# Kernel optimization log

Hardware: AMD Instinct MI355X
Metric: run time of the kernel (lower is better)

The kernel has to match this reference:

```python
import jax, jax.numpy as jnp
import numpy as np

IN_FEATURES = 512
OUT_FEATURES = 512
GRID_SIZE = 5
SPLINE_ORDER = 3
GRID_RANGE = (-3.0, 3.0)


def make_grid():
    h = (GRID_RANGE[1] - GRID_RANGE[0]) / GRID_SIZE
    g = jnp.arange(-SPLINE_ORDER, GRID_SIZE + SPLINE_ORDER + 1, dtype=jnp.float32) * h + GRID_RANGE[0]
    return jnp.broadcast_to(g, (IN_FEATURES, g.shape[0]))  # [in, grid_size+2*order+1]


def b_splines(x, grid):
    # x: [N, in] -> bases: [N, in, grid_size + spline_order]
    x = x[..., None]  # [N, in, 1]
    bases = ((x >= grid[:, :-1]) & (x < grid[:, 1:])).astype(x.dtype)
    for k in range(1, SPLINE_ORDER + 1):
        left = (x - grid[:, :-(k + 1)]) / (grid[:, k:-1] - grid[:, :-(k + 1)])
        right = (grid[:, k + 1:] - x) / (grid[:, k + 1:] - grid[:, 1:-k])
        bases = left * bases[..., :-1] + right * bases[..., 1:]
    return bases


def setup_inputs() -> dict:
    key = jax.random.key(0)
    k1, k2, k3, k4 = jax.random.split(key, 4)
    N = 32768
    bound = 1.0 / np.sqrt(IN_FEATURES)  # kaiming_uniform-ish scale
    x = jax.random.normal(k1, (N, IN_FEATURES), dtype=jnp.float32)
    base_weight = jax.random.uniform(k2, (OUT_FEATURES, IN_FEATURES), minval=-bound, maxval=bound, dtype=jnp.float32)
    spline_weight = jax.random.normal(k3, (OUT_FEATURES, IN_FEATURES, GRID_SIZE + SPLINE_ORDER), dtype=jnp.float32) * 0.1
    spline_scaler = jax.random.uniform(k4, (OUT_FEATURES, IN_FEATURES), minval=-bound, maxval=bound, dtype=jnp.float32)
    grid = make_grid()
    return {"x": x, "base_weight": base_weight, "spline_weight": spline_weight, "spline_scaler": spline_scaler, "grid": grid}


def reference(x, base_weight, spline_weight, spline_scaler, grid):
    # base branch: SiLU(x) @ W_base^T
    base_out = jnp.einsum('ni,oi->no', jax.nn.silu(x), base_weight)
    # spline branch: Cox-de Boor basis then GEMM with scaled spline weights
    b = b_splines(x, grid)  # [N, in, G+K]
    sw = spline_weight * spline_scaler[..., None]  # [out, in, G+K]
    spline_out = jnp.einsum('nik,oik->no', b, sw)
    return base_out + spline_out
```

## Files before the change

kernel.cpp:

```cpp
#include <hip/hip_runtime.h>

#define NSAMP 32768
#define INF 512
#define OUTF 512
#define NB 8
#define KSP 4096
#define KTOT 4608

typedef __attribute__((ext_vector_type(8))) short bf16x8;
typedef __attribute__((ext_vector_type(4))) float f32x4;

typedef __attribute__((address_space(1))) void gas_void;
typedef __attribute__((address_space(3))) void las_void;
#define GLL16(g, l) __builtin_amdgcn_global_load_lds( \
    (const gas_void*)(g), (las_void*)(l), 16, 0, 0)

__device__ __forceinline__ unsigned short f2bf(float f) {
  unsigned int u = __float_as_uint(f);
  u += 0x7fffu + ((u >> 16) & 1u);
  return (unsigned short)(u >> 16);
}

__device__ __forceinline__ unsigned pack_rn(float lo, float hi) {
  return __builtin_amdgcn_perm(__float_as_uint(hi) + 0x8000u,
                               __float_as_uint(lo) + 0x8000u, 0x07060302u);
}

__device__ __forceinline__ uint4 kan_basis_vec(float xv) {
  float t = __builtin_fmaf(xv, 1.0f / 1.2f, 5.5f);
  float cf = floorf(t);
  float u = t - cf;
  int j0 = (int)cf - 3;
  float omu = 1.0f - u;
  float u2 = u * u, u3 = u2 * u;
  float omu2 = omu * omu;
  float w0 = omu2 * omu;
  float w1 = __builtin_fmaf(3.f, u3, __builtin_fmaf(-6.f, u2, 4.f));
  float w2 = __builtin_fmaf(-3.f, u3,
              __builtin_fmaf(3.f, u2, __builtin_fmaf(3.f, u, 1.f)));
  float w3 = u3;
  unsigned P0 = pack_rn(w0, w1);
  unsigned P1 = pack_rn(w2, w3);
  int p = j0 & 1;
  unsigned Q0 = p ? (P0 << 16) : P0;
  unsigned Q1 = p ? __builtin_amdgcn_alignbit(P1, P0, 16) : P1;
  unsigned Q2 = p ? (P1 >> 16) : 0u;
  int D = j0 >> 1;
  uint4 r;
  r.x = (D == 0) ? Q0 : (D == -1) ? Q1 : (D == -2) ? Q2 : 0u;
  r.y = (D == 1) ? Q0 : (D ==  0) ? Q1 : (D == -1) ? Q2 : 0u;
  r.z = (D == 2) ? Q0 : (D ==  1) ? Q1 : (D ==  0) ? Q2 : 0u;
  r.w = (D == 3) ? Q0 : (D ==  2) ? Q1 : (D ==  1) ? Q2 : 0u;
  return r;
}

__global__ __launch_bounds__(256) void kan_prep_w(
    const float* __restrict__ bw, const float* __restrict__ sw,
    const float* __restrict__ sc, unsigned short* __restrict__ W) {
  int idx = blockIdx.x * 256 + threadIdx.x;
  float scv = sc[idx] * (1.0f / 6.0f);
  float4 s0 = ((const float4*)sw)[idx * 2 + 0];
  float4 s1 = ((const float4*)sw)[idx * 2 + 1];
  unsigned short v[8];
  v[0] = f2bf(s0.x * scv); v[1] = f2bf(s0.y * scv);
  v[2] = f2bf(s0.z * scv); v[3] = f2bf(s0.w * scv);
  v[4] = f2bf(s1.x * scv); v[5] = f2bf(s1.y * scv);
  v[6] = f2bf(s1.z * scv); v[7] = f2bf(s1.w * scv);
  int o = idx >> 9, i = idx & 511;
  *(bf16x8*)(W + (size_t)o * KTOT + i * NB) = *(bf16x8*)v;
  W[(size_t)o * KTOT + KSP + i] = f2bf(bw[idx]);
}

__device__ __forceinline__ void mfma16(
    f32x4 acc[4][8], const bf16x8 av[4], const bf16x8 bv[4], int nh) {
  #pragma unroll
  for (int mf = 0; mf < 4; ++mf)
    #pragma unroll
    for (int g = 0; g < 4; ++g)
      acc[mf][nh * 4 + g] = __builtin_amdgcn_mfma_f32_16x16x32_bf16(
          av[mf], bv[g], acc[mf][nh * 4 + g], 0, 0, 0);
}

__global__ __launch_bounds__(256, 2) void kan_fused(
    const float* __restrict__ x, const unsigned short* __restrict__ W,
    float* __restrict__ out) {
  __shared__ __align__(16) unsigned short As[128 * 64];
  __shared__ __align__(16) unsigned short Bs[2][256 * 64];
  const int tid = threadIdx.x;
  const int wave = tid >> 6;
  const int lane = tid & 63;
  const int frow = lane & 15;
  const int quad = lane >> 4;
  const int lr = lane >> 3;
  const int lc = lane & 7;
  const int mtile = blockIdx.x & 255;
  const int ntile = blockIdx.x >> 8;
  const int wm = (wave & 1) << 6;
  const int wn = (wave >> 1) << 7;
  const int fr7 = frow & 7;
  const int sa0 = (quad ^ fr7) * 8;
  const int sa1 = ((4 + quad) ^ fr7) * 8;

  f32x4 acc[4][8];
  #pragma unroll
  for (int i = 0; i < 4; ++i)
    #pragma unroll
    for (int j = 0; j < 8; ++j)
      acc[i][j] = (f32x4){0.f, 0.f, 0.f, 0.f};

  const unsigned short* bg = W +
      (size_t)(ntile * 256 + wave * 64 + lr) * KTOT + ((lc ^ lr) * 8);
  const float* xb = x + (size_t)mtile * 128 * INF;
  const float* xp[4];
  #pragma unroll
  for (int is = 0; is < 4; ++is)
    xp[is] = xb + (size_t)(wave * 32 + is * 8 + lr) * INF + lc;

  {
    float xc[4];
    #pragma unroll
    for (int is = 0; is < 4; ++is) xc[is] = xp[is][0];
    #pragma unroll
    for (int is = 0; is < 8; ++is)
      GLL16(bg + is * 36864, &Bs[0][(wave * 64 + is * 8) * 64]);
    bg += 64;
    #pragma unroll
    for (int is = 0; is < 4; ++is) {
      uint4 bb = kan_basis_vec(xc[is]);
      *(uint4*)&As[(wave * 32 + is * 8 + lr) * 64 + ((lc ^ lr) * 8)] = bb;
    }
    asm volatile("s_waitcnt vmcnt(0)");
    __syncthreads();
  }

  for (int kc = 0; kc < 72; ++kc) {
    const unsigned short* Bc = Bs[kc & 1];
    unsigned short* Bn = (unsigned short*)Bs[(kc + 1) & 1];
    bf16x8 av[4], bv[4];
    float xn[4];
    float4 v0[4], v1[4];

    if (kc < 63) {
      #pragma unroll
      for (int is = 0; is < 4; ++is) xn[is] = xp[is][(kc + 1) * 8];
    }
    if (kc < 71) {
      #pragma unroll
      for (int is = 0; is < 8; ++is)
        GLL16(bg + is * 36864, &Bn[(wave * 64 + is * 8) * 64]);
      bg += 64;
    }
    #pragma unroll
    for (int f = 0; f < 4; ++f)
      av[f] = *(const bf16x8*)&As[(wm + f * 16 + frow) * 64 + sa0];
    #pragma unroll
    for (int g = 0; g < 4; ++g)
      bv[g] = *(const bf16x8*)&Bc[(wn + g * 16 + frow) * 64 + sa0];
    __builtin_amdgcn_s_barrier();
    asm volatile("s_waitcnt lgkmcnt(0)");
    __builtin_amdgcn_sched_barrier(0);
    __builtin_amdgcn_s_setprio(1);
    mfma16(acc, av, bv, 0);
    __builtin_amdgcn_s_setprio(0);
    __builtin_amdgcn_s_barrier();

    #pragma unroll
    for (int g = 0; g < 4; ++g)
      bv[g] = *(const bf16x8*)&Bc[(wn + (g + 4) * 16 + frow) * 64 + sa0];
    __builtin_amdgcn_s_barrier();
    asm volatile("s_waitcnt lgkmcnt(0)");
    __builtin_amdgcn_sched_barrier(0);
    __builtin_amdgcn_s_setprio(1);
    mfma16(acc, av, bv, 1);
    __builtin_amdgcn_s_setprio(0);
    __builtin_amdgcn_s_barrier();

    if (kc >= 63 && kc < 71) {
      const int scn = kc - 63;
      #pragma unroll
      for (int is = 0; is < 4; ++is) {
        const float* xr =
            xb + (size_t)(wave * 32 + is * 8 + lr) * INF + scn * 64 + lc * 8;
        v0[is] = *(const float4*)xr;
        v1[is] = *(const float4*)(xr + 4);
      }
    }
    #pragma unroll
    for (int f = 0; f < 4; ++f)
      av[f] = *(const bf16x8*)&As[(wm + f * 16 + frow) * 64 + sa1];
    #pragma unroll
    for (int g = 0; g < 4; ++g)
      bv[g] = *(const bf16x8*)&Bc[(wn + g * 16 + frow) * 64 + sa1];
    __builtin_amdgcn_s_barrier();
    asm volatile("s_waitcnt lgkmcnt(0)");
    __builtin_amdgcn_sched_barrier(0);
    __builtin_amdgcn_s_setprio(1);
    mfma16(acc, av, bv, 0);
    __builtin_amdgcn_s_setprio(0);
    __builtin_amdgcn_s_barrier();

    #pragma unroll
    for (int g = 0; g < 4; ++g)
      bv[g] = *(const bf16x8*)&Bc[(wn + (g + 4) * 16 + frow) * 64 + sa1];
    if (kc < 63) {
      #pragma unroll
      for (int is = 0; is < 4; ++is) {
        uint4 bb = kan_basis_vec(xn[is]);
        *(uint4*)&As[(wave * 32 + is * 8 + lr) * 64 + ((lc ^ lr) * 8)] = bb;
      }
    } else if (kc < 71) {
      #pragma unroll
      for (int is = 0; is < 4; ++is) {
        float vv[8] = {v0[is].x, v0[is].y, v0[is].z, v0[is].w,
                       v1[is].x, v1[is].y, v1[is].z, v1[is].w};
        float s[8];
        #pragma unroll
        for (int e = 0; e < 8; ++e)
          s[e] = vv[e] * __builtin_amdgcn_rcpf(1.0f + __expf(-vv[e]));
        uint4 pk;
        pk.x = pack_rn(s[0], s[1]);
        pk.y = pack_rn(s[2], s[3]);
        pk.z = pack_rn(s[4], s[5]);
        pk.w = pack_rn(s[6], s[7]);
        *(uint4*)&As[(wave * 32 + is * 8 + lr) * 64 + ((lc ^ lr) * 8)] = pk;
      }
    }
    if (kc < 71)
      asm volatile("s_waitcnt vmcnt(0)");
    __builtin_amdgcn_s_barrier();
    asm volatile("s_waitcnt lgkmcnt(0)");
    __builtin_amdgcn_sched_barrier(0);
    __builtin_amdgcn_s_setprio(1);
    mfma16(acc, av, bv, 1);
    __builtin_amdgcn_s_setprio(0);
    __builtin_amdgcn_s_barrier();
  }

  const size_t m0 = (size_t)mtile * 128;
  const int n0 = ntile * 256;
  #pragma unroll
  for (int mf = 0; mf < 4; ++mf)
    #pragma unroll
    for (int nf = 0; nf < 8; ++nf)
      #pragma unroll
      for (int r = 0; r < 4; ++r)
        out[(m0 + wm + mf * 16 + quad * 4 + r) * OUTF + (n0 + wn + nf * 16 + frow)] =
            acc[mf][nf][r];
}

__global__ __launch_bounds__(256) void kan_naive(
    const float* __restrict__ x, const float* __restrict__ bw,
    const float* __restrict__ sw, const float* __restrict__ sc,
    float* __restrict__ out) {
  int idx = blockIdx.x * 256 + threadIdx.x;
  int n = idx >> 9, o = idx & 511;
  const float* xr = x + (size_t)n * INF;
  float acc = 0.f;
  for (int i = 0; i < INF; ++i) {
    float xv = xr[i];
    float sil = xv / (1.0f + __expf(-xv));
    float t = (xv + 6.6f) * (1.0f / 1.2f);
    float cf = floorf(t);
    float u = t - cf;
    int j0 = (int)cf - 3;
    float omu = 1.0f - u;
    float u2 = u * u, u3 = u2 * u;
    float w[4];
    w[0] = (1.0f / 6.0f) * omu * omu * omu;
    w[1] = (1.0f / 6.0f) * (3.0f * u3 - 6.0f * u2 + 4.0f);
    w[2] = (1.0f / 6.0f) * (-3.0f * u3 + 3.0f * u2 + 3.0f * u + 1.0f);
    w[3] = (1.0f / 6.0f) * u3;
    int wi = o * INF + i;
    acc += sil * bw[wi];
    float sp = 0.f;
    #pragma unroll
    for (int m = 0; m < 4; ++m) {
      int j = j0 + m;
      if ((unsigned)j < 8u) sp += w[m] * sw[wi * NB + j];
    }
    acc += sp * sc[wi];
  }
  out[idx] = acc;
}

extern "C" void kernel_launch(void* const* d_in, const int* in_sizes, int n_in,
                              void* d_out, int out_size, void* d_ws, size_t ws_size,
                              hipStream_t stream) {
  const float* x  = (const float*)d_in[0];
  const float* bw = (const float*)d_in[1];
  const float* sw = (const float*)d_in[2];
  const float* sc = (const float*)d_in[3];
  float* out = (float*)d_out;

  const size_t wbytes = (size_t)OUTF * KTOT * 2;
  if (ws_size >= wbytes) {
    unsigned short* W = (unsigned short*)d_ws;
    kan_prep_w<<<(OUTF * INF) / 256, 256, 0, stream>>>(bw, sw, sc, W);
    kan_fused<<<(NSAMP / 128) * (OUTF / 256), 256, 0, stream>>>(x, W, out);
  } else {
    kan_naive<<<(NSAMP * OUTF) / 256, 256, 0, stream>>>(x, bw, sw, sc, out);
  }
}
```

Baseline: 268.7 us.

## Enlarge fused KAN GEMM tile to 256x256 with 8 waves and double-buffered A

The fused kernel moves from 128x256 tiles with 4 waves to 256x256 tiles with 8 waves (512 threads). Each wave now computes a 128x64 sub-tile, and the A tile (spline basis / SiLU values) is double-buffered in shared memory. Basis computation and B-tile global-to-LDS loads are spread across the four MFMA phases of each K step. The aim is more reuse of each loaded W tile, fewer blocks, and better overlap of basis generation with MFMA. The cost is 64KB of LDS per block, which likely limits occupancy below the declared two blocks per CU, plus heavier per-thread register pressure.

```diff
diff --git a/kernel.cpp b/kernel.cpp
--- a/kernel.cpp
+++ b/kernel.cpp
@@ -72,19 +72,19 @@
 }
 
 __device__ __forceinline__ void mfma16(
-    f32x4 acc[4][8], const bf16x8 av[4], const bf16x8 bv[4], int nh) {
+    f32x4 acc[8][4], int mbase, const bf16x8 av[4], const bf16x8 bv[4]) {
   #pragma unroll
   for (int mf = 0; mf < 4; ++mf)
     #pragma unroll
     for (int g = 0; g < 4; ++g)
-      acc[mf][nh * 4 + g] = __builtin_amdgcn_mfma_f32_16x16x32_bf16(
-          av[mf], bv[g], acc[mf][nh * 4 + g], 0, 0, 0);
-}
-
-__global__ __launch_bounds__(256, 2) void kan_fused(
+      acc[mbase + mf][g] = __builtin_amdgcn_mfma_f32_16x16x32_bf16(
+          av[mf], bv[g], acc[mbase + mf][g], 0, 0, 0);
+}
+
+__global__ __launch_bounds__(512, 2) void kan_fused(
     const float* __restrict__ x, const unsigned short* __restrict__ W,
     float* __restrict__ out) {
-  __shared__ __align__(16) unsigned short As[128 * 64];
+  __shared__ __align__(16) unsigned short As[2][256 * 64];
   __shared__ __align__(16) unsigned short Bs[2][256 * 64];
   const int tid = threadIdx.x;
   const int wave = tid >> 6;
@@ -93,159 +93,194 @@
   const int quad = lane >> 4;
   const int lr = lane >> 3;
   const int lc = lane & 7;
-  const int mtile = blockIdx.x & 255;
-  const int ntile = blockIdx.x >> 8;
-  const int wm = (wave & 1) << 6;
-  const int wn = (wave >> 1) << 7;
+  const int mtile = blockIdx.x & 127;
+  const int ntile = blockIdx.x >> 7;
+  const int wm = (wave & 1) << 7;
+  const int wn = (wave >> 1) << 6;
   const int fr7 = frow & 7;
   const int sa0 = (quad ^ fr7) * 8;
   const int sa1 = ((4 + quad) ^ fr7) * 8;
 
-  f32x4 acc[4][8];
+  f32x4 acc[8][4];
   #pragma unroll
-  for (int i = 0; i < 4; ++i)
-    #pragma unroll
-    for (int j = 0; j < 8; ++j)
+  for (int i = 0; i < 8; ++i)
+    #pragma unroll
+    for (int j = 0; j < 4; ++j)
       acc[i][j] = (f32x4){0.f, 0.f, 0.f, 0.f};
 
   const unsigned short* bg = W +
-      (size_t)(ntile * 256 + wave * 64 + lr) * KTOT + ((lc ^ lr) * 8);
-  const float* xb = x + (size_t)mtile * 128 * INF;
-  const float* xp[4];
-  #pragma unroll
-  for (int is = 0; is < 4; ++is)
-    xp[is] = xb + (size_t)(wave * 32 + is * 8 + lr) * INF + lc;
+      (size_t)(ntile * 256 + wave * 8 + lr) * KTOT + ((lc ^ lr) * 8);
+  const float* xb = x + (size_t)mtile * 256 * INF;
+  const int rt = tid >> 1;
+  const int half = tid & 1;
+  const int rt7 = rt & 7;
+  const float* xs_sp = xb + (size_t)rt * INF + half * 4;
+  const float* xs_si = xb + (size_t)rt * INF + half * 32;
 
   {
-    float xc[4];
-    #pragma unroll
-    for (int is = 0; is < 4; ++is) xc[is] = xp[is][0];
-    #pragma unroll
-    for (int is = 0; is < 8; ++is)
-      GLL16(bg + is * 36864, &Bs[0][(wave * 64 + is * 8) * 64]);
+    float4 xv = *(const float4*)xs_sp;
+    #pragma unroll
+    for (int ir = 0; ir < 4; ++ir)
+      GLL16(bg + (size_t)ir * (64 * KTOT), &Bs[0][(ir * 64 + wave * 8) * 64]);
     bg += 64;
-    #pragma unroll
-    for (int is = 0; is < 4; ++is) {
-      uint4 bb = kan_basis_vec(xc[is]);
-      *(uint4*)&As[(wave * 32 + is * 8 + lr) * 64 + ((lc ^ lr) * 8)] = bb;
-    }
-    asm volatile("s_waitcnt vmcnt(0)");
+    float xe[4] = {xv.x, xv.y, xv.z, xv.w};
+    #pragma unroll
+    for (int e = 0; e < 4; ++e) {
+      uint4 bb = kan_basis_vec(xe[e]);
+      *(uint4*)&As[0][rt * 64 + (((half * 4 + e) ^ rt7) * 8)] = bb;
+    }
     __syncthreads();
   }
 
-  for (int kc = 0; kc < 72; ++kc) {
-    const unsigned short* Bc = Bs[kc & 1];
-    unsigned short* Bn = (unsigned short*)Bs[(kc + 1) & 1];
-    bf16x8 av[4], bv[4];
-    float xn[4];
-    float4 v0[4], v1[4];
-
-    if (kc < 63) {
+  for (int k = 0; k < 72; ++k) {
+    const unsigned short* Ac = As[k & 1];
+    const unsigned short* Bc = Bs[k & 1];
+    unsigned short* An = As[(k + 1) & 1];
+    unsigned short* Bn = Bs[(k + 1) & 1];
+    const bool spl = (k < 63);
+    const bool sil = (k >= 63) && (k < 71);
+    const int scn = k - 63;
+
+    bf16x8 avA[4], avB[4], bvA[4], bvB[4];
+    float4 xv;
+    float4 xq0[4];
+
+    if (spl) {
+      xv = *(const float4*)(xs_sp + (size_t)(k + 1) * 8);
+    } else if (sil) {
+      const float* xr = xs_si + scn * 64;
+      xq0[0] = *(const float4*)(xr + 0);
+      xq0[1] = *(const float4*)(xr + 4);
+      xq0[2] = *(const float4*)(xr + 8);
+      xq0[3] = *(const float4*)(xr + 12);
+    }
+    if (k < 71) {
+      GLL16(bg, &Bn[(wave * 8) * 64]);
+      GLL16(bg + (size_t)(64 * KTOT), &Bn[(64 + wave * 8) * 64]);
+    }
+    #pragma unroll
+    for (int f = 0; f < 4; ++f)
+      avA[f] = *(const bf16x8*)&Ac[(wm + f * 16 + frow) * 64 + sa0];
+    #pragma unroll
+    for (int g = 0; g < 4; ++g)
+      bvA[g] = *(const bf16x8*)&Bc[(wn + g * 16 + frow) * 64 + sa0];
+    __builtin_amdgcn_sched_barrier(0);
+    __builtin_amdgcn_s_barrier();
+    asm volatile("s_waitcnt lgkmcnt(0)");
+    __builtin_amdgcn_sched_barrier(0);
+    __builtin_amdgcn_s_setprio(1);
+    mfma16(acc, 0, avA, bvA);
+    __builtin_amdgcn_s_setprio(0);
+    __builtin_amdgcn_s_barrier();
+
+    if (k < 71)
+      GLL16(bg + (size_t)(128 * KTOT), &Bn[(128 + wave * 8) * 64]);
+    if (spl) {
+      uint4 b0 = kan_basis_vec(xv.x);
+      uint4 b1 = kan_basis_vec(xv.y);
+      *(uint4*)&An[rt * 64 + (((half * 4 + 0) ^ rt7) * 8)] = b0;
+      *(uint4*)&An[rt * 64 + (((half * 4 + 1) ^ rt7) * 8)] = b1;
+    } else if (sil) {
+      float a[16] = {xq0[0].x, xq0[0].y, xq0[0].z, xq0[0].w,
+                     xq0[1].x, xq0[1].y, xq0[1].z, xq0[1].w,
+                     xq0[2].x, xq0[2].y, xq0[2].z, xq0[2].w,
+                     xq0[3].x, xq0[3].y, xq0[3].z, xq0[3].w};
+      float sl[16];
       #pragma unroll
-      for (int is = 0; is < 4; ++is) xn[is] = xp[is][(kc + 1) * 8];
-    }
-    if (kc < 71) {
+      for (int e = 0; e < 16; ++e)
+        sl[e] = a[e] * __builtin_amdgcn_rcpf(1.0f + __expf(-a[e]));
+      uint4 p0, p1;
+      p0.x = pack_rn(sl[0], sl[1]);   p0.y = pack_rn(sl[2], sl[3]);
+      p0.z = pack_rn(sl[4], sl[5]);   p0.w = pack_rn(sl[6], sl[7]);
+      p1.x = pack_rn(sl[8], sl[9]);   p1.y = pack_rn(sl[10], sl[11]);
+      p1.z = pack_rn(sl[12], sl[13]); p1.w = pack_rn(sl[14], sl[15]);
+      *(uint4*)&An[rt * 64 + (((half * 4 + 0) ^ rt7) * 8)] = p0;
+      *(uint4*)&An[rt * 64 + (((half * 4 + 1) ^ rt7) * 8)] = p1;
+    }
+    #pragma unroll
+    for (int f = 0; f < 4; ++f)
+      avB[f] = *(const bf16x8*)&Ac[(wm + (f + 4) * 16 + frow) * 64 + sa0];
+    __builtin_amdgcn_sched_barrier(0);
+    __builtin_amdgcn_s_barrier();
+    asm volatile("s_waitcnt lgkmcnt(0)");
+    __builtin_amdgcn_sched_barrier(0);
+    __builtin_amdgcn_s_setprio(1);
+    mfma16(acc, 4, avB, bvA);
+    __builtin_amdgcn_s_setprio(0);
+    __builtin_amdgcn_s_barrier();
+
+    float4 xq1[4];
+    if (k < 71)
+      GLL16(bg + (size_t)(192 * KTOT), &Bn[(192 + wave * 8) * 64]);
+    if (sil) {
+      const float* xr = xs_si + scn * 64 + 16;
+      xq1[0] = *(const float4*)(xr + 0);
+      xq1[1] = *(const float4*)(xr + 4);
+      xq1[2] = *(const float4*)(xr + 8);
+      xq1[3] = *(const float4*)(xr + 12);
+    }
+    #pragma unroll
+    for (int f = 0; f < 4; ++f)
+      avA[f] = *(const bf16x8*)&Ac[(wm + f * 16 + frow) * 64 + sa1];
+    #pragma unroll
+    for (int g = 0; g < 4; ++g)
+      bvB[g] = *(const bf16x8*)&Bc[(wn + g * 16 + frow) * 64 + sa1];
+    __builtin_amdgcn_sched_barrier(0);
+    __builtin_amdgcn_s_barrier();
+    asm volatile("s_waitcnt lgkmcnt(0)");
+    __builtin_amdgcn_sched_barrier(0);
+    __builtin_amdgcn_s_setprio(1);
+    mfma16(acc, 0, avA, bvB);
+    __builtin_amdgcn_s_setprio(0);
+    __builtin_amdgcn_s_barrier();
+
+    if (spl) {
+      uint4 b2 = kan_basis_vec(xv.z);
+      uint4 b3 = kan_basis_vec(xv.w);
+      *(uint4*)&An[rt * 64 + (((half * 4 + 2) ^ rt7) * 8)] = b2;
+      *(uint4*)&An[rt * 64 + (((half * 4 + 3) ^ rt7) * 8)] = b3;
+    } else if (sil) {
+      float a[16] = {xq1[0].x, xq1[0].y, xq1[0].z, xq1[0].w,
+                     xq1[1].x, xq1[1].y, xq1[1].z, xq1[1].w,
+                     xq1[2].x, xq1[2].y, xq1[2].z, xq1[2].w,
+                     xq1[3].x, xq1[3].y, xq1[3].z, xq1[3].w};
+      float sl[16];
       #pragma unroll
-      for (int is = 0; is < 8; ++is)
-        GLL16(bg + is * 36864, &Bn[(wave * 64 + is * 8) * 64]);
-      bg += 64;
+      for (int e = 0; e < 16; ++e)
+        sl[e] = a[e] * __builtin_amdgcn_rcpf(1.0f + __expf(-a[e]));
+      uint4 p2, p3;
+      p2.x = pack_rn(sl[0], sl[1]);   p2.y = pack_rn(sl[2], sl[3]);
+      p2.z = pack_rn(sl[4], sl[5]);   p2.w = pack_rn(sl[6], sl[7]);
+      p3.x = pack_rn(sl[8], sl[9]);   p3.y = pack_rn(sl[10], sl[11]);
+      p3.z = pack_rn(sl[12], sl[13]); p3.w = pack_rn(sl[14], sl[15]);
+      *(uint4*)&An[rt * 64 + (((half * 4 + 2) ^ rt7) * 8)] = p2;
+      *(uint4*)&An[rt * 64 + (((half * 4 + 3) ^ rt7) * 8)] = p3;
     }
     #pragma unroll
     for (int f = 0; f < 4; ++f)
-      av[f] = *(const bf16x8*)&As[(wm + f * 16 + frow) * 64 + sa0];
-    #pragma unroll
-    for (int g = 0; g < 4; ++g)
-      bv[g] = *(const bf16x8*)&Bc[(wn + g * 16 + frow) * 64 + sa0];
-    __builtin_amdgcn_s_barrier();
-    asm volatile("s_waitcnt lgkmcnt(0)");
+      avB[f] = *(const bf16x8*)&Ac[(wm + (f + 4) * 16 + frow) * 64 + sa1];
+    asm volatile("s_waitcnt vmcnt(0) lgkmcnt(0)");
+    __builtin_amdgcn_sched_barrier(0);
+    __builtin_amdgcn_s_barrier();
     __builtin_amdgcn_sched_barrier(0);
     __builtin_amdgcn_s_setprio(1);
-    mfma16(acc, av, bv, 0);
+    mfma16(acc, 4, avB, bvB);
     __builtin_amdgcn_s_setprio(0);
     __builtin_amdgcn_s_barrier();
 
-    #pragma unroll
-    for (int g = 0; g < 4; ++g)
-      bv[g] = *(const bf16x8*)&Bc[(wn + (g + 4) * 16 + frow) * 64 + sa0];
-    __builtin_amdgcn_s_barrier();
-    asm volatile("s_waitcnt lgkmcnt(0)");
-    __builtin_amdgcn_sched_barrier(0);
-    __builtin_amdgcn_s_setprio(1);
-    mfma16(acc, av, bv, 1);
-    __builtin_amdgcn_s_setprio(0);
-    __builtin_amdgcn_s_barrier();
-
-    if (kc >= 63 && kc < 71) {
-      const int scn = kc - 63;
-      #pragma unroll
-      for (int is = 0; is < 4; ++is) {
-        const float* xr =
-            xb + (size_t)(wave * 32 + is * 8 + lr) * INF + scn * 64 + lc * 8;
-        v0[is] = *(const float4*)xr;
-        v1[is] = *(const float4*)(xr + 4);
-      }
-    }
-    #pragma unroll
-    for (int f = 0; f < 4; ++f)
-      av[f] = *(const bf16x8*)&As[(wm + f * 16 + frow) * 64 + sa1];
-    #pragma unroll
-    for (int g = 0; g < 4; ++g)
-      bv[g] = *(const bf16x8*)&Bc[(wn + g * 16 + frow) * 64 + sa1];
-    __builtin_amdgcn_s_barrier();
-    asm volatile("s_waitcnt lgkmcnt(0)");
-    __builtin_amdgcn_sched_barrier(0);
-    __builtin_amdgcn_s_setprio(1);
-    mfma16(acc, av, bv, 0);
-    __builtin_amdgcn_s_setprio(0);
-    __builtin_amdgcn_s_barrier();
-
-    #pragma unroll
-    for (int g = 0; g < 4; ++g)
-      bv[g] = *(const bf16x8*)&Bc[(wn + (g + 4) * 16 + frow) * 64 + sa1];
-    if (kc < 63) {
-      #pragma unroll
-      for (int is = 0; is < 4; ++is) {
-        uint4 bb = kan_basis_vec(xn[is]);
-        *(uint4*)&As[(wave * 32 + is * 8 + lr) * 64 + ((lc ^ lr) * 8)] = bb;
-      }
-    } else if (kc < 71) {
-      #pragma unroll
-      for (int is = 0; is < 4; ++is) {
-        float vv[8] = {v0[is].x, v0[is].y, v0[is].z, v0[is].w,
-                       v1[is].x, v1[is].y, v1[is].z, v1[is].w};
-        float s[8];
-        #pragma unroll
-        for (int e = 0; e < 8; ++e)
-          s[e] = vv[e] * __builtin_amdgcn_rcpf(1.0f + __expf(-vv[e]));
-        uint4 pk;
-        pk.x = pack_rn(s[0], s[1]);
-        pk.y = pack_rn(s[2], s[3]);
-        pk.z = pack_rn(s[4], s[5]);
-        pk.w = pack_rn(s[6], s[7]);
-        *(uint4*)&As[(wave * 32 + is * 8 + lr) * 64 + ((lc ^ lr) * 8)] = pk;
-      }
-    }
-    if (kc < 71)
-      asm volatile("s_waitcnt vmcnt(0)");
-    __builtin_amdgcn_s_barrier();
-    asm volatile("s_waitcnt lgkmcnt(0)");
-    __builtin_amdgcn_sched_barrier(0);
-    __builtin_amdgcn_s_setprio(1);
-    mfma16(acc, av, bv, 1);
-    __builtin_amdgcn_s_setprio(0);
-    __builtin_amdgcn_s_barrier();
+    bg += 64;
   }
 
-  const size_t m0 = (size_t)mtile * 128;
+  const size_t m0 = (size_t)mtile * 256;
   const int n0 = ntile * 256;
   #pragma unroll
-  for (int mf = 0; mf < 4; ++mf)
-    #pragma unroll
-    for (int nf = 0; nf < 8; ++nf)
+  for (int mf = 0; mf < 8; ++mf)
+    #pragma unroll
+    for (int nf = 0; nf < 4; ++nf)
       #pragma unroll
       for (int r = 0; r < 4; ++r)
-        out[(m0 + wm + mf * 16 + quad * 4 + r) * OUTF + (n0 + wn + nf * 16 + frow)] =
-            acc[mf][nf][r];
+        out[(m0 + wm + mf * 16 + quad * 4 + r) * OUTF +
+            (n0 + wn + nf * 16 + frow)] = acc[mf][nf][r];
 }
 
 __global__ __launch_bounds__(256) void kan_naive(
@@ -296,7 +331,7 @@
   if (ws_size >= wbytes) {
     unsigned short* W = (unsigned short*)d_ws;
     kan_prep_w<<<(OUTF * INF) / 256, 256, 0, stream>>>(bw, sw, sc, W);
-    kan_fused<<<(NSAMP / 128) * (OUTF / 256), 256, 0, stream>>>(x, W, out);
+    kan_fused<<<(NSAMP / 256) * (OUTF / 256), 512, 0, stream>>>(x, W, out);
   } else {
     kan_naive<<<(NSAMP * OUTF) / 256, 256, 0, stream>>>(x, bw, sw, sc, out);
   }
```

Measured after the change: 337.3 us. 25.6% more time.
